# Optimization experiments

Hardware: AMD Instinct MI355X
Metric: run time of the kernel (lower is better)

The kernel has to match this reference:

```python
import jax, jax.numpy as jnp
import numpy as np

N = 100000
D = 128
E = 500000
R = 3


def _sage_conv(x, edge_index, Wl, bl, Wr):
    # PyG SAGEConv, mean aggregation:
    #   out = lin_l(mean_{j in N(i)} x_j) + lin_r(x_i)
    src, dst = edge_index[0], edge_index[1]
    msg = x[src]                                             # [E, D] gather
    summed = jax.ops.segment_sum(msg, dst, num_segments=N)   # [N, D] scatter-add
    cnt = jax.ops.segment_sum(jnp.ones((msg.shape[0],), x.dtype), dst, num_segments=N)
    agg = summed / jnp.maximum(cnt, 1.0)[:, None]            # mean (0 if no neighbors)
    return agg @ Wl + bl + x @ Wr


def setup_inputs() -> dict:
    key = jax.random.key(0)
    ks = jax.random.split(key, 10)
    s = 1.0 / np.sqrt(D)
    return {
        "x": jax.random.normal(ks[0], (N, D), jnp.float32),
        "edge_index_0": jax.random.randint(ks[1], (2, E), 0, N),
        "edge_index_1": jax.random.randint(ks[2], (2, E), 0, N),
        "edge_index_2": jax.random.randint(ks[3], (2, E), 0, N),
        "W_l": jax.random.normal(ks[4], (R, D, D), jnp.float32) * s,
        "b_l": jnp.zeros((R, D), jnp.float32),
        "W_r": jax.random.normal(ks[5], (R, D, D), jnp.float32) * s,
        "P1": jax.random.normal(ks[6], (R * D, D), jnp.float32) * (1.0 / np.sqrt(R * D)),
        "b1": jnp.zeros((D,), jnp.float32),
        "P2": jax.random.normal(ks[7], (D, D), jnp.float32) * s,
        "b2": jnp.zeros((D,), jnp.float32),
    }


def reference(x, edge_index_0, edge_index_1, edge_index_2, W_l, b_l, W_r, P1, b1, P2, b2):
    edges = (edge_index_0, edge_index_1, edge_index_2)
    rel_embs = [_sage_conv(x, edges[r], W_l[r], b_l[r], W_r[r]) for r in range(R)]
    combined = jnp.concatenate(rel_embs, axis=-1)            # [N, R*D]
    h = jax.nn.relu(combined @ P1 + b1)                       # [N, D]
    return h @ P2 + b2
```

## Files before the change

kernel.cpp:

```cpp
#include <hip/hip_runtime.h>
#include <hip/hip_bf16.h>

#define NN 100000
#define DD 128
#define EE 500000
#define RR 3
#define MM (RR * NN)
#define NBIN 293
#define BCAP_RAW 6144
#define BCAP_PAD 10240

typedef __attribute__((ext_vector_type(8))) short   bf16x8;
typedef __attribute__((ext_vector_type(8))) ushort  ushort8;
typedef __attribute__((ext_vector_type(4))) float   f32x4;
typedef __attribute__((ext_vector_type(2))) unsigned uintx2;

__device__ __forceinline__ ushort f2bf(float f) {
    __hip_bfloat16 h = __float2bfloat16(f);
    return *(ushort*)&h;
}
__device__ __forceinline__ float bflo(unsigned v) {
    unsigned u = v << 16;
    return *(float*)&u;
}
__device__ __forceinline__ float bfhi(unsigned v) {
    unsigned u = v & 0xffff0000u;
    return *(float*)&u;
}

__global__ __launch_bounds__(128) void precompute_qbt_kernel(
    const float* __restrict__ Wl, const float* __restrict__ Wr,
    const float* __restrict__ P1, ushort* __restrict__ QBt)
{
    int s = blockIdx.x >> 7;
    int i = blockIdx.x & 127;
    int j = threadIdx.x;
    float acc = 0.f;
    if (s == 0) {
        for (int r = 0; r < RR; ++r) {
            const float* wrow = Wr + (size_t)(r * DD + i) * DD;
            const float* pcol = P1 + (size_t)(r * DD) * DD + j;
            for (int k = 0; k < DD; ++k)
                acc += wrow[k] * pcol[(size_t)k * DD];
        }
    } else {
        int r = s - 1;
        const float* wrow = Wl + (size_t)(r * DD + i) * DD;
        const float* pcol = P1 + (size_t)(r * DD) * DD + j;
        for (int k = 0; k < DD; ++k)
            acc += wrow[k] * pcol[(size_t)k * DD];
    }
    QBt[(size_t)j * 512 + s * DD + i] = f2bf(acc);
}

__global__ __launch_bounds__(128) void precompute_p2t_kernel(
    const float* __restrict__ P2, ushort* __restrict__ P2t)
{
    int j = blockIdx.x;
    int k = threadIdx.x;
    P2t[(size_t)j * DD + k] = f2bf(P2[(size_t)k * DD + j]);
}

__global__ __launch_bounds__(128) void precompute_c_kernel(
    const float* __restrict__ bl, const float* __restrict__ P1,
    const float* __restrict__ b1, float* __restrict__ cb)
{
    int j = threadIdx.x;
    float acc = b1[j];
    for (int r = 0; r < RR; ++r)
        for (int k = 0; k < DD; ++k)
            acc += bl[r * DD + k] * P1[(size_t)(r * DD + k) * DD + j];
    cb[j] = acc;
}

__global__ __launch_bounds__(256) void x_tobf16_kernel(
    const float* __restrict__ x, ushort* __restrict__ xh)
{
    size_t i = (size_t)blockIdx.x * 256 + threadIdx.x;
    if (i * 4 >= (size_t)NN * DD) return;
    float4 v = ((const float4*)x)[i];
    unsigned lo = (unsigned)f2bf(v.x) | ((unsigned)f2bf(v.y) << 16);
    unsigned hi = (unsigned)f2bf(v.z) | ((unsigned)f2bf(v.w) << 16);
    ((uint2*)xh)[i] = make_uint2(lo, hi);
}

__global__ __launch_bounds__(256) void bin_kernel(
    const int* __restrict__ e0, const int* __restrict__ e1, const int* __restrict__ e2,
    int* __restrict__ g_cursor, int* __restrict__ g_bindata)
{
    __shared__ int hist[NBIN];
    __shared__ int base[NBIN];
    int tid = threadIdx.x;
    for (int i = tid; i < NBIN; i += 256) hist[i] = 0;
    __syncthreads();
    int e_begin = blockIdx.x * 4096;
    int e_end = e_begin + 4096; if (e_end > RR * EE) e_end = RR * EE;
    for (int i = e_begin + tid; i < e_end; i += 256) {
        int r = i / EE, e = i - r * EE;
        const int* ei = (r == 0) ? e0 : (r == 1) ? e1 : e2;
        int bin = (r * NN + ei[EE + e]) >> 10;
        atomicAdd(&hist[bin], 1);
    }
    __syncthreads();
    for (int i = tid; i < NBIN; i += 256) {
        int c = hist[i];
        base[i] = c ? atomicAdd(&g_cursor[i], c) : 0;
        hist[i] = 0;
    }
    __syncthreads();
    for (int i = e_begin + tid; i < e_end; i += 256) {
        int r = i / EE, e = i - r * EE;
        const int* ei = (r == 0) ? e0 : (r == 1) ? e1 : e2;
        int src = ei[e];
        int b = r * NN + ei[EE + e];
        int bin = b >> 10, local = b & 1023;
        int slot = base[bin] + atomicAdd(&hist[bin], 1);
        if (slot < BCAP_RAW) g_bindata[(size_t)bin * BCAP_RAW + slot] = src | (local << 17);
    }
}

__global__ __launch_bounds__(256) void sort_kernel(
    const int* __restrict__ g_cursor, const int* __restrict__ g_bindata,
    int* __restrict__ sorted, uint2* __restrict__ meta)
{
    __shared__ int hist[1024];
    __shared__ int start[1024];
    __shared__ int ssum[256];
    int bin = blockIdx.x, tid = threadIdx.x;
    int cnt = g_cursor[bin]; if (cnt > BCAP_RAW) cnt = BCAP_RAW;
    const int* bd = g_bindata + (size_t)bin * BCAP_RAW;
    for (int i = tid; i < 1024; i += 256) hist[i] = 0;
    __syncthreads();
    for (int i = tid; i < cnt; i += 256)
        atomicAdd(&hist[bd[i] >> 17], 1);
    __syncthreads();
    int t4 = tid * 4;
    int a0 = hist[t4], a1 = hist[t4 + 1], a2 = hist[t4 + 2], a3 = hist[t4 + 3];
    int p0 = (a0 + 7) & ~7, p1 = (a1 + 7) & ~7, p2 = (a2 + 7) & ~7, p3 = (a3 + 7) & ~7;
    int ts = p0 + p1 + p2 + p3;
    ssum[tid] = ts;
    __syncthreads();
    #pragma unroll
    for (int off = 1; off < 256; off <<= 1) {
        int tmp = (tid >= off) ? ssum[tid - off] : 0;
        __syncthreads();
        ssum[tid] += tmp;
        __syncthreads();
    }
    int ex = ssum[tid] - ts;
    start[t4] = ex; start[t4 + 1] = ex + p0;
    start[t4 + 2] = ex + p0 + p1; start[t4 + 3] = ex + p0 + p1 + p2;
    __syncthreads();
    for (int i = tid; i < 1024; i += 256) {
        int bucket = (bin << 10) + i;
        if (bucket < MM)
            meta[bucket] = make_uint2((unsigned)(bin * BCAP_PAD + start[i]),
                                      (unsigned)hist[i]);
        hist[i] = start[i];
    }
    __syncthreads();
    int* sb = sorted + (size_t)bin * BCAP_PAD;
    for (int i = tid; i < cnt; i += 256) {
        int w = bd[i];
        int pos = atomicAdd(&hist[w >> 17], 1);
        if (pos < BCAP_PAD) sb[pos] = w & 0x1ffff;
    }
    __syncthreads();
    for (int i = tid; i < 1024; i += 256) {
        int s0 = start[i];
        int d = hist[i] - s0;
        int pl = (d + 7) & ~7;
        for (int p = s0 + d; p < s0 + pl; ++p)
            if (p < BCAP_PAD) sb[p] = NN;
    }
}

__global__ __launch_bounds__(256) void aggregate_kernel(
    const ushort* __restrict__ xh, const int* __restrict__ sorted,
    const uint2* __restrict__ meta, ushort* __restrict__ aggh)
{
    int grp = blockIdx.x * 4 + (threadIdx.x >> 6);
    int lane = threadIdx.x & 63;
    int bid0 = grp * 4;
    uintx2 m = __builtin_nontemporal_load(
        (const uintx2*)meta + (bid0 + (lane & 3)));
    int st[4], dg[4];
    #pragma unroll
    for (int b = 0; b < 4; ++b) {
        st[b] = __builtin_amdgcn_readlane((int)m.x, b);
        dg[b] = __builtin_amdgcn_readlane((int)m.y, b);
    }
    int start0 = st[0];
    int L = (st[3] - start0) + ((dg[3] + 7) & ~7);
    const unsigned* xu = (const unsigned*)xh;
    float ax[4], ay[4];
    #pragma unroll
    for (int b = 0; b < 4; ++b) { ax[b] = 0.f; ay[b] = 0.f; }

    if (L <= 64) {
        int sidx = __builtin_nontemporal_load(&sorted[start0 + lane]);
        #pragma unroll
        for (int b = 0; b < 4; ++b) {
            int off = st[b] - start0;
            int degp = (dg[b] + 7) & ~7;
            for (int j = 0; j < degp; j += 8) {
                #pragma unroll
                for (int u = 0; u < 8; ++u) {
                    int sj = __builtin_amdgcn_readlane(sidx, off + j + u);
                    unsigned v = xu[(size_t)sj * 64 + lane];
                    ax[b] += bflo(v);
                    ay[b] += bfhi(v);
                }
            }
        }
    } else {
        #pragma unroll
        for (int b = 0; b < 4; ++b) {
            const int* sb = sorted + st[b];
            int degp = (dg[b] + 7) & ~7;
            for (int j = 0; j < degp; j += 8) {
                #pragma unroll
                for (int u = 0; u < 8; ++u) {
                    int sj = sb[j + u];
                    unsigned v = xu[(size_t)sj * 64 + lane];
                    ax[b] += bflo(v);
                    ay[b] += bfhi(v);
                }
            }
        }
    }
    #pragma unroll
    for (int b = 0; b < 4; ++b) {
        int deg = dg[b];
        float sc = 1.0f / (float)(deg > 1 ? deg : 1);
        unsigned o = (unsigned)f2bf(ax[b] * sc) | ((unsigned)f2bf(ay[b] * sc) << 16);
        ((unsigned*)(aggh + (size_t)(bid0 + b) * DD))[lane] = o;
    }
}

__global__ __launch_bounds__(256) void gemm_fused_kernel(
    const ushort* __restrict__ xh, const ushort* __restrict__ aggh,
    const ushort* __restrict__ QBt, const float* __restrict__ cb,
    const ushort* __restrict__ P2t, const float* __restrict__ b2,
    float* __restrict__ out)
{
    __shared__ ushort S[18432];
    ushort (*As)[72]  = (ushort(*)[72])S;
    ushort (*Bs)[72]  = (ushort(*)[72])(S + 9216);
    ushort (*Hs)[136] = (ushort(*)[136])S;

    int tid = threadIdx.x;
    int n0 = blockIdx.x * 128;
    int wid = tid >> 6;
    int lane = tid & 63;
    int wr = wid >> 1, wc = wid & 1;
    int lrow = lane & 15;
    int lk = (lane >> 4) * 8;

    f32x4 acc[4][4];
    #pragma unroll
    for (int i = 0; i < 4; ++i)
        #pragma unroll
        for (int j = 0; j < 4; ++j) acc[i][j] = (f32x4){0.f, 0.f, 0.f, 0.f};

    for (int c = 0; c < 8; ++c) {
        int seg = c >> 1;
        int kloc = (c & 1) * 64;
        const ushort* Abase = (seg == 0) ? xh : (aggh + (size_t)(seg - 1) * NN * DD);
        if (c) __syncthreads();
        #pragma unroll
        for (int i = 0; i < 4; ++i) {
            int id = tid + i * 256;
            int row = id >> 3;
            int s16 = id & 7;
            int grow = n0 + row;
            ushort8 v = {0, 0, 0, 0, 0, 0, 0, 0};
            if (grow < NN)
                v = *(const ushort8*)(Abase + (size_t)grow * DD + kloc + s16 * 8);
            *(ushort8*)&As[row][s16 * 8] = v;
        }
        #pragma unroll
        for (int i = 0; i < 4; ++i) {
            int id = tid + i * 256;
            int n = id >> 3;
            int s16 = id & 7;
            *(ushort8*)&Bs[n][s16 * 8] =
                *(const ushort8*)(QBt + (size_t)n * 512 + c * 64 + s16 * 8);
        }
        __syncthreads();
        #pragma unroll
        for (int ks = 0; ks < 2; ++ks) {
            bf16x8 a[4], b[4];
            #pragma unroll
            for (int mi = 0; mi < 4; ++mi)
                a[mi] = *(const bf16x8*)&As[wr * 64 + mi * 16 + lrow][ks * 32 + lk];
            #pragma unroll
            for (int ni = 0; ni < 4; ++ni)
                b[ni] = *(const bf16x8*)&Bs[wc * 64 + ni * 16 + lrow][ks * 32 + lk];
            #pragma unroll
            for (int mi = 0; mi < 4; ++mi)
                #pragma unroll
                for (int ni = 0; ni < 4; ++ni)
                    acc[mi][ni] = __builtin_amdgcn_mfma_f32_16x16x32_bf16(
                        a[mi], b[ni], acc[mi][ni], 0, 0, 0);
        }
    }

    bf16x8 pb[4][4];
    #pragma unroll
    for (int ks = 0; ks < 4; ++ks)
        #pragma unroll
        for (int ni = 0; ni < 4; ++ni)
            pb[ks][ni] = *(const bf16x8*)(P2t +
                (size_t)(wc * 64 + ni * 16 + lrow) * DD + ks * 32 + lk);

    __syncthreads();

    int crow = lane >> 4;
    int ccol = lane & 15;
    #pragma unroll
    for (int ni = 0; ni < 4; ++ni) {
        int gcol = wc * 64 + ni * 16 + ccol;
        float cv = cb[gcol];
        #pragma unroll
        for (int mi = 0; mi < 4; ++mi) {
            #pragma unroll
            for (int q = 0; q < 4; ++q) {
                float v = acc[mi][ni][q] + cv;
                v = v > 0.f ? v : 0.f;
                Hs[wr * 64 + mi * 16 + crow * 4 + q][gcol] = f2bf(v);
            }
        }
    }
    __syncthreads();

    f32x4 acc2[4][4];
    #pragma unroll
    for (int i = 0; i < 4; ++i)
        #pragma unroll
        for (int j = 0; j < 4; ++j) acc2[i][j] = (f32x4){0.f, 0.f, 0.f, 0.f};

    #pragma unroll
    for (int ks = 0; ks < 4; ++ks) {
        bf16x8 a[4];
        #pragma unroll
        for (int mi = 0; mi < 4; ++mi)
            a[mi] = *(const bf16x8*)&Hs[wr * 64 + mi * 16 + lrow][ks * 32 + lk];
        #pragma unroll
        for (int mi = 0; mi < 4; ++mi)
            #pragma unroll
            for (int ni = 0; ni < 4; ++ni)
                acc2[mi][ni] = __builtin_amdgcn_mfma_f32_16x16x32_bf16(
                    a[mi], pb[ks][ni], acc2[mi][ni], 0, 0, 0);
    }

    #pragma unroll
    for (int ni = 0; ni < 4; ++ni) {
        int gcol = wc * 64 + ni * 16 + ccol;
        float bv = b2[gcol];
        #pragma unroll
        for (int mi = 0; mi < 4; ++mi) {
            #pragma unroll
            for (int q = 0; q < 4; ++q) {
                int gr = n0 + wr * 64 + mi * 16 + crow * 4 + q;
                if (gr < NN)
                    __builtin_nontemporal_store(acc2[mi][ni][q] + bv,
                                                &out[(size_t)gr * DD + gcol]);
            }
        }
    }
}

extern "C" void kernel_launch(void* const* d_in, const int* in_sizes, int n_in,
                              void* d_out, int out_size, void* d_ws, size_t ws_size,
                              hipStream_t stream) {
    const float* x  = (const float*)d_in[0];
    const int*   e0 = (const int*)d_in[1];
    const int*   e1 = (const int*)d_in[2];
    const int*   e2 = (const int*)d_in[3];
    const float* Wl = (const float*)d_in[4];
    const float* bl = (const float*)d_in[5];
    const float* Wr = (const float*)d_in[6];
    const float* P1 = (const float*)d_in[7];
    const float* b1 = (const float*)d_in[8];
    const float* P2 = (const float*)d_in[9];
    const float* b2 = (const float*)d_in[10];
    float* out = (float*)d_out;

    ushort* xh       = (ushort*)d_ws;
    ushort* aggh     = xh + (size_t)(NN + 1) * DD;
    ushort* QBt      = aggh + (size_t)RR * NN * DD;
    ushort* P2t      = QBt + (size_t)128 * 512;
    float*  cb       = (float*)(P2t + (size_t)DD * DD);
    int*    g_cursor = (int*)(cb + DD);
    int*    g_bindat = g_cursor + NBIN;
    int*    sorted   = g_bindat + (size_t)NBIN * BCAP_RAW;
    uint2*  meta     = (uint2*)(sorted + (size_t)NBIN * BCAP_PAD + 64);

    (void)hipMemsetAsync(g_cursor, 0, NBIN * sizeof(int), stream);
    (void)hipMemsetAsync(xh + (size_t)NN * DD, 0, DD * sizeof(ushort), stream);

    precompute_qbt_kernel<<<4 * DD, DD, 0, stream>>>(Wl, Wr, P1, QBt);
    precompute_p2t_kernel<<<DD, DD, 0, stream>>>(P2, P2t);
    precompute_c_kernel<<<1, DD, 0, stream>>>(bl, P1, b1, cb);

    x_tobf16_kernel<<<(NN * DD / 4 + 255) / 256, 256, 0, stream>>>(x, xh);

    int ablocks = (RR * EE + 4095) / 4096;
    bin_kernel<<<ablocks, 256, 0, stream>>>(e0, e1, e2, g_cursor, g_bindat);

    sort_kernel<<<NBIN, 256, 0, stream>>>(g_cursor, g_bindat, sorted, meta);

    aggregate_kernel<<<MM / 16, 256, 0, stream>>>(xh, sorted, meta, aggh);

    int gblocks = (NN + 127) / 128;
    gemm_fused_kernel<<<gblocks, 256, 0, stream>>>(xh, aggh, QBt, cb, P2t, b2, out);
}
```

Measured before the change: 210.7 us.

## Fuse neighbor mean aggregation into the GEMM kernel via shared-memory A tiles

Removes the separate aggregate kernel and the global aggh buffer. The fused GEMM kernel now gathers and averages neighbor rows for each relation straight into a 128x128 bf16 shared-memory tile, then runs MFMA against the matching QBt slice. This avoids writing and re-reading 3*N*D bf16 of aggregated features and one kernel launch. In exchange, the irregular gather latency now sits inside the GEMM blocks with extra synchronization, shared memory per block grows, and only about 782 blocks are available to hide that latency.

```diff
diff --git a/kernel.cpp b/kernel.cpp
--- a/kernel.cpp
+++ b/kernel.cpp
@@ -175,79 +175,15 @@
     }
 }
 
-__global__ __launch_bounds__(256) void aggregate_kernel(
+__global__ __launch_bounds__(256, 3) void gemm_fused_kernel(
     const ushort* __restrict__ xh, const int* __restrict__ sorted,
-    const uint2* __restrict__ meta, ushort* __restrict__ aggh)
-{
-    int grp = blockIdx.x * 4 + (threadIdx.x >> 6);
-    int lane = threadIdx.x & 63;
-    int bid0 = grp * 4;
-    uintx2 m = __builtin_nontemporal_load(
-        (const uintx2*)meta + (bid0 + (lane & 3)));
-    int st[4], dg[4];
-    #pragma unroll
-    for (int b = 0; b < 4; ++b) {
-        st[b] = __builtin_amdgcn_readlane((int)m.x, b);
-        dg[b] = __builtin_amdgcn_readlane((int)m.y, b);
-    }
-    int start0 = st[0];
-    int L = (st[3] - start0) + ((dg[3] + 7) & ~7);
-    const unsigned* xu = (const unsigned*)xh;
-    float ax[4], ay[4];
-    #pragma unroll
-    for (int b = 0; b < 4; ++b) { ax[b] = 0.f; ay[b] = 0.f; }
-
-    if (L <= 64) {
-        int sidx = __builtin_nontemporal_load(&sorted[start0 + lane]);
-        #pragma unroll
-        for (int b = 0; b < 4; ++b) {
-            int off = st[b] - start0;
-            int degp = (dg[b] + 7) & ~7;
-            for (int j = 0; j < degp; j += 8) {
-                #pragma unroll
-                for (int u = 0; u < 8; ++u) {
-                    int sj = __builtin_amdgcn_readlane(sidx, off + j + u);
-                    unsigned v = xu[(size_t)sj * 64 + lane];
-                    ax[b] += bflo(v);
-                    ay[b] += bfhi(v);
-                }
-            }
-        }
-    } else {
-        #pragma unroll
-        for (int b = 0; b < 4; ++b) {
-            const int* sb = sorted + st[b];
-            int degp = (dg[b] + 7) & ~7;
-            for (int j = 0; j < degp; j += 8) {
-                #pragma unroll
-                for (int u = 0; u < 8; ++u) {
-                    int sj = sb[j + u];
-                    unsigned v = xu[(size_t)sj * 64 + lane];
-                    ax[b] += bflo(v);
-                    ay[b] += bfhi(v);
-                }
-            }
-        }
-    }
-    #pragma unroll
-    for (int b = 0; b < 4; ++b) {
-        int deg = dg[b];
-        float sc = 1.0f / (float)(deg > 1 ? deg : 1);
-        unsigned o = (unsigned)f2bf(ax[b] * sc) | ((unsigned)f2bf(ay[b] * sc) << 16);
-        ((unsigned*)(aggh + (size_t)(bid0 + b) * DD))[lane] = o;
-    }
-}
-
-__global__ __launch_bounds__(256) void gemm_fused_kernel(
-    const ushort* __restrict__ xh, const ushort* __restrict__ aggh,
-    const ushort* __restrict__ QBt, const float* __restrict__ cb,
-    const ushort* __restrict__ P2t, const float* __restrict__ b2,
-    float* __restrict__ out)
-{
-    __shared__ ushort S[18432];
-    ushort (*As)[72]  = (ushort(*)[72])S;
-    ushort (*Bs)[72]  = (ushort(*)[72])(S + 9216);
-    ushort (*Hs)[136] = (ushort(*)[136])S;
+    const uint2* __restrict__ meta, const ushort* __restrict__ QBt,
+    const float* __restrict__ cb, const ushort* __restrict__ P2t,
+    const float* __restrict__ b2, float* __restrict__ out)
+{
+    __shared__ ushort S[26624];
+    ushort (*At)[136] = (ushort(*)[136])S;
+    ushort (*Bs)[72]  = (ushort(*)[72])(S + 17408);
 
     int tid = threadIdx.x;
     int n0 = blockIdx.x * 128;
@@ -256,6 +192,7 @@
     int wr = wid >> 1, wc = wid & 1;
     int lrow = lane & 15;
     int lk = (lane >> 4) * 8;
+    const unsigned* xu = (const unsigned*)xh;
 
     f32x4 acc[4][4];
     #pragma unroll
@@ -263,46 +200,110 @@
         #pragma unroll
         for (int j = 0; j < 4; ++j) acc[i][j] = (f32x4){0.f, 0.f, 0.f, 0.f};
 
-    for (int c = 0; c < 8; ++c) {
-        int seg = c >> 1;
-        int kloc = (c & 1) * 64;
-        const ushort* Abase = (seg == 0) ? xh : (aggh + (size_t)(seg - 1) * NN * DD);
-        if (c) __syncthreads();
-        #pragma unroll
-        for (int i = 0; i < 4; ++i) {
-            int id = tid + i * 256;
-            int row = id >> 3;
-            int s16 = id & 7;
-            int grow = n0 + row;
-            ushort8 v = {0, 0, 0, 0, 0, 0, 0, 0};
-            if (grow < NN)
-                v = *(const ushort8*)(Abase + (size_t)grow * DD + kloc + s16 * 8);
-            *(ushort8*)&As[row][s16 * 8] = v;
+    for (int seg = 0; seg < 4; ++seg) {
+        if (seg) __syncthreads();
+        if (seg == 0) {
+            #pragma unroll
+            for (int i = 0; i < 8; ++i) {
+                int id = tid + i * 256;
+                int row = id >> 4, cc = id & 15;
+                int grow = n0 + row;
+                ushort8 v = {0, 0, 0, 0, 0, 0, 0, 0};
+                if (grow < NN)
+                    v = *(const ushort8*)(xh + (size_t)grow * DD + cc * 8);
+                *(ushort8*)&At[row][cc * 8] = v;
+            }
+        } else {
+            int r = seg - 1;
+            for (int g = 0; g < 8; ++g) {
+                int row0 = wid * 32 + g * 4;
+                int gbase = n0 + row0;
+                int bid0 = r * NN + gbase;
+                int mIdx = bid0 + (lane & 3);
+                if (mIdx > MM - 1) mIdx = MM - 1;
+                uintx2 m = __builtin_nontemporal_load((const uintx2*)meta + mIdx);
+                int st[4], dg[4];
+                #pragma unroll
+                for (int b = 0; b < 4; ++b) {
+                    st[b] = __builtin_amdgcn_readlane((int)m.x, b);
+                    dg[b] = __builtin_amdgcn_readlane((int)m.y, b);
+                    if (gbase + b >= NN) dg[b] = 0;
+                }
+                int start0 = st[0];
+                int L = (st[3] - start0) + ((dg[3] + 7) & ~7);
+                float ax[4], ay[4];
+                #pragma unroll
+                for (int b = 0; b < 4; ++b) { ax[b] = 0.f; ay[b] = 0.f; }
+                bool tail = (gbase + 3 >= NN);
+                if (L <= 64 && !tail) {
+                    int sidx = __builtin_nontemporal_load(&sorted[start0 + lane]);
+                    #pragma unroll
+                    for (int b = 0; b < 4; ++b) {
+                        int off = st[b] - start0;
+                        int degp = (dg[b] + 7) & ~7;
+                        for (int j = 0; j < degp; j += 8) {
+                            #pragma unroll
+                            for (int u = 0; u < 8; ++u) {
+                                int sj = __builtin_amdgcn_readlane(sidx, off + j + u);
+                                unsigned v = xu[(size_t)sj * 64 + lane];
+                                ax[b] += bflo(v);
+                                ay[b] += bfhi(v);
+                            }
+                        }
+                    }
+                } else {
+                    #pragma unroll
+                    for (int b = 0; b < 4; ++b) {
+                        const int* sb = sorted + st[b];
+                        int degp = (dg[b] + 7) & ~7;
+                        for (int j = 0; j < degp; j += 8) {
+                            #pragma unroll
+                            for (int u = 0; u < 8; ++u) {
+                                int sj = sb[j + u];
+                                unsigned v = xu[(size_t)sj * 64 + lane];
+                                ax[b] += bflo(v);
+                                ay[b] += bfhi(v);
+                            }
+                        }
+                    }
+                }
+                #pragma unroll
+                for (int b = 0; b < 4; ++b) {
+                    int deg = dg[b];
+                    float sc = 1.0f / (float)(deg > 1 ? deg : 1);
+                    unsigned o = (unsigned)f2bf(ax[b] * sc) |
+                                 ((unsigned)f2bf(ay[b] * sc) << 16);
+                    ((unsigned*)&At[row0 + b][0])[lane] = o;
+                }
+            }
         }
         #pragma unroll
-        for (int i = 0; i < 4; ++i) {
-            int id = tid + i * 256;
-            int n = id >> 3;
-            int s16 = id & 7;
-            *(ushort8*)&Bs[n][s16 * 8] =
-                *(const ushort8*)(QBt + (size_t)n * 512 + c * 64 + s16 * 8);
-        }
-        __syncthreads();
-        #pragma unroll
-        for (int ks = 0; ks < 2; ++ks) {
-            bf16x8 a[4], b[4];
-            #pragma unroll
-            for (int mi = 0; mi < 4; ++mi)
-                a[mi] = *(const bf16x8*)&As[wr * 64 + mi * 16 + lrow][ks * 32 + lk];
-            #pragma unroll
-            for (int ni = 0; ni < 4; ++ni)
-                b[ni] = *(const bf16x8*)&Bs[wc * 64 + ni * 16 + lrow][ks * 32 + lk];
-            #pragma unroll
-            for (int mi = 0; mi < 4; ++mi)
+        for (int kc = 0; kc < 2; ++kc) {
+            __syncthreads();
+            #pragma unroll
+            for (int i = 0; i < 4; ++i) {
+                int id = tid + i * 256;
+                int n = id >> 3, s16 = id & 7;
+                *(ushort8*)&Bs[n][s16 * 8] =
+                    *(const ushort8*)(QBt + (size_t)n * 512 + seg * 128 + kc * 64 + s16 * 8);
+            }
+            __syncthreads();
+            #pragma unroll
+            for (int ks2 = 0; ks2 < 2; ++ks2) {
+                bf16x8 a[4], b[4];
+                #pragma unroll
+                for (int mi = 0; mi < 4; ++mi)
+                    a[mi] = *(const bf16x8*)&At[wr * 64 + mi * 16 + lrow][kc * 64 + ks2 * 32 + lk];
                 #pragma unroll
                 for (int ni = 0; ni < 4; ++ni)
-                    acc[mi][ni] = __builtin_amdgcn_mfma_f32_16x16x32_bf16(
-                        a[mi], b[ni], acc[mi][ni], 0, 0, 0);
+                    b[ni] = *(const bf16x8*)&Bs[wc * 64 + ni * 16 + lrow][ks2 * 32 + lk];
+                #pragma unroll
+                for (int mi = 0; mi < 4; ++mi)
+                    #pragma unroll
+                    for (int ni = 0; ni < 4; ++ni)
+                        acc[mi][ni] = __builtin_amdgcn_mfma_f32_16x16x32_bf16(
+                            a[mi], b[ni], acc[mi][ni], 0, 0, 0);
+            }
         }
     }
 
@@ -328,7 +329,7 @@
             for (int q = 0; q < 4; ++q) {
                 float v = acc[mi][ni][q] + cv;
                 v = v > 0.f ? v : 0.f;
-                Hs[wr * 64 + mi * 16 + crow * 4 + q][gcol] = f2bf(v);
+                At[wr * 64 + mi * 16 + crow * 4 + q][gcol] = f2bf(v);
             }
         }
     }
@@ -345,7 +346,7 @@
         bf16x8 a[4];
         #pragma unroll
         for (int mi = 0; mi < 4; ++mi)
-            a[mi] = *(const bf16x8*)&Hs[wr * 64 + mi * 16 + lrow][ks * 32 + lk];
+            a[mi] = *(const bf16x8*)&At[wr * 64 + mi * 16 + lrow][ks * 32 + lk];
         #pragma unroll
         for (int mi = 0; mi < 4; ++mi)
             #pragma unroll
@@ -388,8 +389,7 @@
     float* out = (float*)d_out;
 
     ushort* xh       = (ushort*)d_ws;
-    ushort* aggh     = xh + (size_t)(NN + 1) * DD;
-    ushort* QBt      = aggh + (size_t)RR * NN * DD;
+    ushort* QBt      = xh + (size_t)(NN + 1) * DD;
     ushort* P2t      = QBt + (size_t)128 * 512;
     float*  cb       = (float*)(P2t + (size_t)DD * DD);
     int*    g_cursor = (int*)(cb + DD);
@@ -411,8 +411,6 @@
 
     sort_kernel<<<NBIN, 256, 0, stream>>>(g_cursor, g_bindat, sorted, meta);
 
-    aggregate_kernel<<<MM / 16, 256, 0, stream>>>(xh, sorted, meta, aggh);
-
     int gblocks = (NN + 127) / 128;
-    gemm_fused_kernel<<<gblocks, 256, 0, stream>>>(xh, aggh, QBt, cb, P2t, b2, out);
-}
+    gemm_fused_kernel<<<gblocks, 256, 0, stream>>>(xh, sorted, meta, QBt, cb, P2t, b2, out);
+}
```

New measurement: 295.1 us. +40.1%, slower.
